# Kernel optimization log

Measured on AMD Instinct MI355X. Metric: run time of the kernel, lower is better.

Reference implementation:

```python
import jax, jax.numpy as jnp
import numpy as np

ALPHA = 0.05          # embed strength (frames in [0,1])
COEF_R, COEF_C = 4, 3 # mid-frequency DCT coefficient that carries the bit


def _dct_mat():
    # 8x8 orthonormal DCT-II matrix
    n = jnp.arange(8, dtype=jnp.float32)
    D = jnp.cos(jnp.pi * (2.0 * n[None, :] + 1.0) * n[:, None] / 16.0) * jnp.sqrt(2.0 / 8.0)
    return D.at[0].multiply(1.0 / jnp.sqrt(2.0))


def rgb_to_yuv(rgb):
    r, g, b = rgb[:, 0:1], rgb[:, 1:2], rgb[:, 2:3]
    y = 0.299 * r + 0.587 * g + 0.114 * b
    u = -0.147 * r - 0.289 * g + 0.436 * b
    v = 0.615 * r - 0.515 * g - 0.1 * b
    return jnp.concatenate([y, u, v], axis=1)


def yuv_to_rgb(yuv):
    y, u, v = yuv[:, 0:1], yuv[:, 1:2], yuv[:, 2:3]
    r = y + 1.14 * v
    g = y - 0.395 * u - 0.581 * v
    b = y + 2.032 * u
    return jnp.concatenate([r, g, b], axis=1)


def lbp_uniform(gray):
    # uniform LBP, P=8, R=1 (integer 8-neighborhood), per-image max-normalized
    B, H, W = gray.shape
    p = jnp.pad(gray, ((0, 0), (1, 1), (1, 1)), mode='edge')
    offs = [(-1, 0), (-1, 1), (0, 1), (1, 1), (1, 0), (1, -1), (0, -1), (-1, -1)]
    neigh = jnp.stack([p[:, 1 + dy:1 + dy + H, 1 + dx:1 + dx + W] for dy, dx in offs], axis=0)
    bits = (neigh >= gray[None]).astype(jnp.float32)          # [8,B,H,W]
    trans = jnp.sum(jnp.abs(bits - jnp.roll(bits, 1, axis=0)), axis=0)
    s = jnp.sum(bits, axis=0)
    code = jnp.where(trans <= 2.0, s, 9.0)
    mx = jnp.max(code, axis=(1, 2), keepdims=True)
    return code / mx                                           # [B,H,W]


def dct_embed(y, watermark, mask):
    # y: [B,H,W] luma; watermark: [L] int bits; mask: [B,H,W] texture strength
    B, H, W = y.shape
    nh, nw = H // 8, W // 8
    D = _dct_mat()
    yb = y.reshape(B, nh, 8, nw, 8).transpose(0, 1, 3, 2, 4)   # [B,nh,nw,8,8]
    coef = jnp.einsum('ij,bhwjk,lk->bhwil', D, yb, D)          # D @ block @ D^T
    strength = mask.reshape(B, nh, 8, nw, 8).mean(axis=(2, 4)) # [B,nh,nw]
    L = watermark.shape[0]
    idx = (jnp.arange(nh * nw) % L).reshape(nh, nw)
    bits = watermark[idx].astype(jnp.float32)                  # [nh,nw]
    delta = ALPHA * strength * (2.0 * bits - 1.0)[None]        # [B,nh,nw]
    coef = coef.at[..., COEF_R, COEF_C].add(delta)
    inv = jnp.einsum('ji,bhwjk,kl->bhwil', D, coef, D)         # D^T @ coef @ D
    return inv.transpose(0, 1, 3, 2, 4).reshape(B, H, W)


def _forward(frame, watermark, sa_w, sa_b, ca_w1, ca_w2):
    # LBP texture features from grayscale
    gray = 0.299 * frame[:, 0] + 0.587 * frame[:, 1] + 0.114 * frame[:, 2]
    lbp = lbp_uniform(gray)[:, None]                           # [B,1,H,W]
    # spatial attention: 7x7 conv over [frame, lbp] -> sigmoid mask
    sa_in = jnp.concatenate([frame, lbp], axis=1)
    mask = jax.nn.sigmoid(
        jax.lax.conv_general_dilated(sa_in, sa_w, (1, 1), 'SAME',
                                     dimension_numbers=('NCHW', 'OIHW', 'NCHW'))
        + sa_b[None, :, None, None])                           # [B,1,H,W]
    # channel attention on YUV
    yuv = rgb_to_yuv(frame)
    pooled = yuv.mean(axis=(2, 3))                             # [B,3]
    scale = jax.nn.sigmoid(jax.nn.relu(pooled @ ca_w1.T) @ ca_w2.T)
    weighted = yuv * scale[:, :, None, None]
    # blockwise DCT watermark embed on Y channel
    y_marked = dct_embed(weighted[:, 0], watermark, mask[:, 0])
    wm_yuv = jnp.concatenate([y_marked[:, None], weighted[:, 1:2], weighted[:, 2:3]], axis=1)
    return yuv_to_rgb(wm_yuv), mask


def setup_inputs() -> dict:
    key = jax.random.key(0)
    k1, k2, k3, k4, k5 = jax.random.split(key, 5)
    B, H, W, L = 16, 512, 512, 64
    frame = jax.random.uniform(k1, (B, 3, H, W), dtype=jnp.float32)
    watermark = jax.random.randint(k2, (L,), 0, 2, dtype=jnp.int32)
    sa_w = jax.random.normal(k3, (1, 4, 7, 7), dtype=jnp.float32) * 0.1
    sa_b = jnp.zeros((1,), dtype=jnp.float32)
    ca_w1 = jax.random.normal(k4, (3, 3), dtype=jnp.float32) * 0.5
    ca_w2 = jax.random.normal(k5, (3, 3), dtype=jnp.float32) * 0.5
    return {"frame": frame, "watermark": watermark, "sa_w": sa_w, "sa_b": sa_b,
            "ca_w1": ca_w1, "ca_w2": ca_w2}


def reference(frame, watermark, sa_w, sa_b, ca_w1, ca_w2):
    return _forward(frame, watermark, sa_w, sa_b, ca_w1, ca_w2)
```

## Files before the change

kernel.cpp:

```cpp
#include <hip/hip_runtime.h>
#include <stdint.h>

#define BB 16
#define HH 512
#define WW 512
#define HWsz (HH*WW)

__device__ __forceinline__ float grayf(float r,float g,float b){
  return __fadd_rn(__fadd_rn(__fmul_rn(0.299f,r),__fmul_rn(0.587f,g)),__fmul_rn(0.114f,b));
}
__device__ __forceinline__ float sigmoidf_(float x){ return 1.0f/(1.0f+expf(-x)); }

__device__ __forceinline__ int lbp_code(float tl,float tc,float tr,
                                        float ml,float c ,float mr,
                                        float bl,float bc,float br){
  int b0 = tc>=c, b1 = tr>=c, b2 = mr>=c, b3 = br>=c;
  int b4 = bc>=c, b5 = bl>=c, b6 = ml>=c, b7 = tl>=c;
  int s = (b0+b1)+(b2+b3)+(b4+b5)+(b6+b7);
  int tr_ = (b0!=b7)+(b1!=b0)+(b2!=b1)+(b3!=b2)+(b4!=b3)+(b5!=b4)+(b6!=b5)+(b7!=b6);
  return (tr_<=2)? s : 9;
}

__global__ void k_init(float* sums, int* maxc){
  int t = threadIdx.x;
  if(t < BB*3) sums[t] = 0.0f;
  if(t < BB) maxc[t] = 0;
}

#define RSTRIDE 520
__global__ __launch_bounds__(256,4) void k_reduce(const float* __restrict__ frame,
     float* __restrict__ sums, int* __restrict__ maxc){
  const int blk = blockIdx.x;
  const int b = blk >> 6;
  const int s = blk & 63;
  const int r0 = s*8;
  const float4* F = (const float4*)(frame + (size_t)b*3*HWsz);
  __shared__ float sg[10*RSTRIDE];
  const int tid = threadIdx.x;
  float sy=0.f, su=0.f, sv=0.f;
  #pragma unroll
  for(int k=0;k<5;k++){
    int j = tid + 256*k;
    int row = j >> 7;
    int c4  = j & 127;
    int gy  = min(max(r0-1+row,0),HH-1);
    int fi  = gy*128 + c4;
    float4 r4 = F[fi];
    float4 g4 = F[65536  + fi];
    float4 b4 = F[131072 + fi];
    float4 gr;
    gr.x = grayf(r4.x,g4.x,b4.x);
    gr.y = grayf(r4.y,g4.y,b4.y);
    gr.z = grayf(r4.z,g4.z,b4.z);
    gr.w = grayf(r4.w,g4.w,b4.w);
    *(float4*)&sg[row*RSTRIDE + 4 + 4*c4] = gr;
    if(c4==0)   sg[row*RSTRIDE + 3]   = gr.x;
    if(c4==127) sg[row*RSTRIDE + 516] = gr.w;
    if(row>=1 && row<=8){
      sy += (gr.x+gr.y)+(gr.z+gr.w);
      float rs_=(r4.x+r4.y)+(r4.z+r4.w), gs_=(g4.x+g4.y)+(g4.z+g4.w), bs_=(b4.x+b4.y)+(b4.z+b4.w);
      su += -0.147f*rs_ - 0.289f*gs_ + 0.436f*bs_;
      sv +=  0.615f*rs_ - 0.515f*gs_ - 0.1f*bs_;
    }
  }
  __syncthreads();
  int cm = 0;
  {
    const float* base = sg + (2*tid + 3);
    float t0=base[0], t1=base[1], t2=base[2], t3=base[3];
    float m0=base[RSTRIDE], m1=base[RSTRIDE+1], m2=base[RSTRIDE+2], m3=base[RSTRIDE+3];
    #pragma unroll
    for(int R=1;R<=8;R++){
      const float* brow = base + (R+1)*RSTRIDE;
      float b0=brow[0], b1=brow[1], b2=brow[2], b3=brow[3];
      cm = max(cm, lbp_code(t0,t1,t2, m0,m1,m2, b0,b1,b2));
      cm = max(cm, lbp_code(t1,t2,t3, m1,m2,m3, b1,b2,b3));
      t0=m0;t1=m1;t2=m2;t3=m3; m0=b0;m1=b1;m2=b2;m3=b3;
    }
  }
  #pragma unroll
  for(int off=32;off>=1;off>>=1){
    sy += __shfl_down(sy,off,64);
    su += __shfl_down(su,off,64);
    sv += __shfl_down(sv,off,64);
    cm = max(cm,__shfl_down(cm,off,64));
  }
  __shared__ float rs[3][4]; __shared__ int rm[4];
  int wave=tid>>6, lane=tid&63;
  if(lane==0){ rs[0][wave]=sy; rs[1][wave]=su; rs[2][wave]=sv; rm[wave]=cm; }
  __syncthreads();
  if(tid==0){
    atomicAdd(&sums[b*3+0], (rs[0][0]+rs[0][1])+(rs[0][2]+rs[0][3]));
    atomicAdd(&sums[b*3+1], (rs[1][0]+rs[1][1])+(rs[1][2]+rs[1][3]));
    atomicAdd(&sums[b*3+2], (rs[2][0]+rs[2][1])+(rs[2][2]+rs[2][3]));
    atomicMax(&maxc[b], max(max(rm[0],rm[1]),max(rm[2],rm[3])));
  }
}

__global__ void k_scale(const float* __restrict__ sums, const int* __restrict__ maxc,
    const float* __restrict__ w1, const float* __restrict__ w2,
    float* __restrict__ scale, float* __restrict__ mxf){
  int b = threadIdx.x;
  if(b >= BB) return;
  float p[3], h[3];
  for(int j=0;j<3;j++) p[j] = sums[b*3+j] * (1.0f/(float)HWsz);
  for(int i=0;i<3;i++){
    float a = p[0]*w1[i*3+0] + p[1]*w1[i*3+1] + p[2]*w1[i*3+2];
    h[i] = fmaxf(a, 0.0f);
  }
  for(int i=0;i<3;i++){
    float a = h[0]*w2[i*3+0] + h[1]*w2[i*3+1] + h[2]*w2[i*3+2];
    scale[b*3+i] = sigmoidf_(a);
  }
  mxf[b] = fmaxf((float)maxc[b], 1.0f);
}

#define SAS 73
__global__ __launch_bounds__(256,3) void k_main(const float* __restrict__ frame,
    const int* __restrict__ wm, const float* __restrict__ sa_w, const float* __restrict__ sa_b,
    const float* __restrict__ scalev, const float* __restrict__ mxf,
    float* __restrict__ out)
{
  const int b = blockIdx.z;
  const int tx0 = blockIdx.x*64, ty0 = blockIdx.y*32;
  const float* fr = frame + (size_t)b*3*HWsz;
  const float4* F4 = (const float4*)fr;

  __shared__ float sA[4][38][SAS];
  __shared__ float sgt[76];
  __shared__ float sgb[76];
  __shared__ float ssc[4];
  __shared__ float scodetab[12];

  const int tid = threadIdx.x;
  if(tid < 3)  ssc[tid] = scalev[b*3 + tid];
  if(tid == 3) ssc[3] = sa_b[0];
  if(tid < 10) scodetab[tid] = (float)tid / mxf[b];

  for(int s = tid; s < 720; s += 256){
    int ly = s / 18;
    int k  = s - ly*18;
    int gy = ty0 + ly - 4;
    int ry = min(max(gy,0),HH-1);
    int gx0 = tx0 + 4*k - 4;
    bool xin = (gx0 >= 0) && (gx0 <= WW-4);
    float4 r4, g4, b4;
    if(xin){
      int fi = ry*(WW/4) + (gx0>>2);
      r4 = F4[fi]; g4 = F4[65536 + fi]; b4 = F4[131072 + fi];
    } else {
      int cc = (gx0 < 0) ? 0 : (WW-1);
      float r = fr[ry*WW+cc], g = fr[HWsz+ry*WW+cc], bl = fr[2*HWsz+ry*WW+cc];
      r4 = make_float4(r,r,r,r); g4 = make_float4(g,g,g,g); b4 = make_float4(bl,bl,bl,bl);
    }
    float gr0 = grayf(r4.x,g4.x,b4.x), gr1 = grayf(r4.y,g4.y,b4.y),
          gr2 = grayf(r4.z,g4.z,b4.z), gr3 = grayf(r4.w,g4.w,b4.w);
    int cbase = 4*k;
    float* gp = (ly==0) ? &sgt[cbase] : ((ly==39) ? &sgb[cbase] : &sA[3][ly-1][cbase]);
    gp[0]=gr0; gp[1]=gr1; gp[2]=gr2; gp[3]=gr3;
    if(ly >= 1 && ly <= 38){
      float z = ((gy >= 0) && (gy < HH) && xin) ? 1.0f : 0.0f;
      float* rp = &sA[0][ly-1][cbase];
      rp[0]          =r4.x*z; rp[1]          =r4.y*z; rp[2]          =r4.z*z; rp[3]          =r4.w*z;
      rp[38*SAS+0]   =g4.x*z; rp[38*SAS+1]   =g4.y*z; rp[38*SAS+2]   =g4.z*z; rp[38*SAS+3]   =g4.w*z;
      rp[2*38*SAS+0] =b4.x*z; rp[2*38*SAS+1] =b4.y*z; rp[2*38*SAS+2] =b4.z*z; rp[2*38*SAS+3] =b4.w*z;
    }
  }
  __syncthreads();

  float lv[3][4];
  #pragma unroll
  for(int it=0; it<3; ++it){
    int s2 = tid + 256*it;
    if(s2 < 684){
      int lr = s2 / 18;
      int q  = s2 - lr*18;
      int lx0 = 4*q;
      const float* rowM = &sA[3][lr][0];
      const float* rowT = (lr==0)  ? sgt : &sA[3][lr-1][0];
      const float* rowB = (lr==37) ? sgb : &sA[3][lr+1][0];
      float t_[6], m_[6], b_[6];
      #pragma unroll
      for(int j=0;j<6;j++){
        int c = lx0 - 1 + j;
        t_[j]=rowT[c]; m_[j]=rowM[c]; b_[j]=rowB[c];
      }
      int gy = ty0 + lr - 3;
      bool rowin = (gy >= 0) && (gy < HH);
      #pragma unroll
      for(int j=0;j<4;j++){
        int lx = lx0 + j;
        int gx = tx0 + lx - 4;
        float v = 0.0f;
        if(rowin && lx >= 1 && lx <= 70 && gx >= 0 && gx < WW){
          float c = m_[j+1];
          int msk = ((t_[j+1]>=c)?1:0)   | ((t_[j+2]>=c)?2:0)  | ((m_[j+2]>=c)?4:0) |
                    ((b_[j+2]>=c)?8:0)   | ((b_[j+1]>=c)?16:0) | ((b_[j]>=c)?32:0)  |
                    ((m_[j]>=c)?64:0)    | ((t_[j]>=c)?128:0);
          int s8  = __popc(msk);
          int rot = ((msk<<1) | (msk>>7)) & 255;
          int tr_ = __popc(msk ^ rot);
          int code = (tr_ <= 2) ? s8 : 9;
          v = scodetab[code];
        }
        lv[it][j] = v;
      }
    }
  }
  __syncthreads();
  #pragma unroll
  for(int it=0; it<3; ++it){
    int s2 = tid + 256*it;
    if(s2 < 684){
      int lr = s2 / 18;
      int q  = s2 - lr*18;
      float* wp2 = &sA[3][lr][4*q];
      wp2[0]=lv[it][0]; wp2[1]=lv[it][1]; wp2[2]=lv[it][2]; wp2[3]=lv[it][3];
    }
  }
  __syncthreads();

  const int t  = tid & 7;
  const int ty = tid >> 3;
  float a0=ssc[3], a1=ssc[3], a2=ssc[3], a3=ssc[3];
  float a4=ssc[3], a5=ssc[3], a6=ssc[3], a7=ssc[3];
  for(int ci=0;ci<4;ci++){
    #pragma unroll
    for(int ky=0;ky<7;ky++){
      const float* rowp = &sA[ci][ty+ky][8*t];
      float win[14];
      #pragma unroll
      for(int w=0;w<14;w++) win[w]=rowp[1+w];
      const float* wr = &sa_w[ci*49 + ky*7];
      #pragma unroll
      for(int kx=0;kx<7;kx++){
        float wt = wr[kx];
        a0 += win[kx+0]*wt;
        a1 += win[kx+1]*wt;
        a2 += win[kx+2]*wt;
        a3 += win[kx+3]*wt;
        a4 += win[kx+4]*wt;
        a5 += win[kx+5]*wt;
        a6 += win[kx+6]*wt;
        a7 += win[kx+7]*wt;
      }
    }
  }
  float m[8];
  m[0]=sigmoidf_(a0); m[1]=sigmoidf_(a1); m[2]=sigmoidf_(a2); m[3]=sigmoidf_(a3);
  m[4]=sigmoidf_(a4); m[5]=sigmoidf_(a5); m[6]=sigmoidf_(a6); m[7]=sigmoidf_(a7);
  {
    size_t midx = (size_t)(3*BB)*HWsz + (size_t)b*HWsz + (size_t)(ty0+ty)*WW + (size_t)(tx0+8*t);
    *reinterpret_cast<float4*>(out + midx)     = make_float4(m[0],m[1],m[2],m[3]);
    *reinterpret_cast<float4*>(out + midx + 4) = make_float4(m[4],m[5],m[6],m[7]);
  }

  float part = ((m[0]+m[1])+(m[2]+m[3])) + ((m[4]+m[5])+(m[6]+m[7]));
  part += __shfl_xor(part, 8, 64);
  part += __shfl_xor(part, 16, 64);
  part += __shfl_xor(part, 32, 64);
  const float strength = part * (1.0f/64.0f);

  {
    const float sc0=ssc[0], sc1=ssc[1], sc2=ssc[2];
    const int bw = (tx0 + 8*t) >> 3;
    const float sgn = (float)(2*wm[bw]-1);
    const float d4 = (((ty+1)&2) ? -0.35355339059327373f : 0.35355339059327373f);
    const float delta = 0.05f * strength * sgn * d4;
    const float D3tab[8] = { 0.4157348061512726f,-0.0975451610080641f,-0.4903926402016152f,-0.2777851165098011f,
                             0.2777851165098011f, 0.4903926402016152f, 0.0975451610080641f,-0.4157348061512726f };
    float vr[8], vg[8], vb[8];
    #pragma unroll
    for(int j=0;j<8;j++){
      float r  = sA[0][ty+3][8*t+j+4];
      float g  = sA[1][ty+3][8*t+j+4];
      float bl = sA[2][ty+3][8*t+j+4];
      float yv = (0.299f*r + 0.587f*g + 0.114f*bl) * sc0;
      float uv = (-0.147f*r - 0.289f*g + 0.436f*bl) * sc1;
      float vv = ( 0.615f*r - 0.515f*g - 0.1f*bl) * sc2;
      float ym = yv + delta * D3tab[j];
      vr[j] = ym + 1.14f*vv;
      vg[j] = ym - 0.395f*uv - 0.581f*vv;
      vb[j] = ym + 2.032f*uv;
    }
    size_t base = (size_t)(ty0+ty)*WW + (size_t)(tx0+8*t);
    float* o0 = out + (size_t)(b*3+0)*HWsz + base;
    float* o1 = out + (size_t)(b*3+1)*HWsz + base;
    float* o2 = out + (size_t)(b*3+2)*HWsz + base;
    *reinterpret_cast<float4*>(o0)   = make_float4(vr[0],vr[1],vr[2],vr[3]);
    *reinterpret_cast<float4*>(o0+4) = make_float4(vr[4],vr[5],vr[6],vr[7]);
    *reinterpret_cast<float4*>(o1)   = make_float4(vg[0],vg[1],vg[2],vg[3]);
    *reinterpret_cast<float4*>(o1+4) = make_float4(vg[4],vg[5],vg[6],vg[7]);
    *reinterpret_cast<float4*>(o2)   = make_float4(vb[0],vb[1],vb[2],vb[3]);
    *reinterpret_cast<float4*>(o2+4) = make_float4(vb[4],vb[5],vb[6],vb[7]);
  }
}

extern "C" void kernel_launch(void* const* d_in, const int* in_sizes, int n_in,
                              void* d_out, int out_size, void* d_ws, size_t ws_size,
                              hipStream_t stream) {
  const float* frame = (const float*)d_in[0];
  const int*   wmark = (const int*)d_in[1];
  const float* sa_w  = (const float*)d_in[2];
  const float* sa_b  = (const float*)d_in[3];
  const float* ca_w1 = (const float*)d_in[4];
  const float* ca_w2 = (const float*)d_in[5];
  float* out = (float*)d_out;
  char* ws = (char*)d_ws;
  float* sums  = (float*)(ws);
  int*   maxc  = (int*)(ws + 192);
  float* scalev= (float*)(ws + 256);
  float* mxf   = (float*)(ws + 448);

  hipLaunchKernelGGL(k_init,  dim3(1),        dim3(64),  0, stream, sums, maxc);
  hipLaunchKernelGGL(k_reduce,dim3(1024),     dim3(256), 0, stream, frame, sums, maxc);
  hipLaunchKernelGGL(k_scale, dim3(1),        dim3(64),  0, stream, sums, maxc, ca_w1, ca_w2, scalev, mxf);
  hipLaunchKernelGGL(k_main,  dim3(8,16,16),  dim3(256), 0, stream, frame, wmark, sa_w, sa_b, scalev, mxf, out);
}
```

Measured before the change: 187.6 us.

## Remap 7x7 conv threads to column-per-thread, 8-row vertical bands

Each thread now owns one column and eight consecutive rows instead of eight horizontal pixels in one row. Every loaded row of 7 taps is reused across up to eight output rows, and the 8x8 block mean becomes a cheap shuffle over eight adjacent lanes. Shared-memory reads become consecutive across lanes, which avoids the stride-8 bank conflicts of the old mapping. In exchange, output stores shrink from float4 vectors to scalar stores, which stay coalesced across the wave, and more FMAs run per loaded value.

```diff
diff --git a/kernel.cpp b/kernel.cpp
--- a/kernel.cpp
+++ b/kernel.cpp
@@ -220,79 +220,76 @@
   }
   __syncthreads();
 
-  const int t  = tid & 7;
-  const int ty = tid >> 3;
-  float a0=ssc[3], a1=ssc[3], a2=ssc[3], a3=ssc[3];
-  float a4=ssc[3], a5=ssc[3], a6=ssc[3], a7=ssc[3];
+  const int x    = tid & 63;
+  const int band = tid >> 6;
+  const int r0s  = band*8;
+  float acc[8];
+  {
+    const float bias = ssc[3];
+    #pragma unroll
+    for(int r=0;r<8;r++) acc[r]=bias;
+  }
   for(int ci=0;ci<4;ci++){
-    #pragma unroll
-    for(int ky=0;ky<7;ky++){
-      const float* rowp = &sA[ci][ty+ky][8*t];
-      float win[14];
+    const float* chan = &sA[ci][0][0] + (r0s)*SAS + (x+1);
+    const float* wci  = &sa_w[ci*49];
+    #pragma unroll
+    for(int i=0;i<14;i++){
+      const float* rowp = chan + i*SAS;
+      float tap[7];
       #pragma unroll
-      for(int w=0;w<14;w++) win[w]=rowp[1+w];
-      const float* wr = &sa_w[ci*49 + ky*7];
+      for(int k=0;k<7;k++) tap[k]=rowp[k];
       #pragma unroll
-      for(int kx=0;kx<7;kx++){
-        float wt = wr[kx];
-        a0 += win[kx+0]*wt;
-        a1 += win[kx+1]*wt;
-        a2 += win[kx+2]*wt;
-        a3 += win[kx+3]*wt;
-        a4 += win[kx+4]*wt;
-        a5 += win[kx+5]*wt;
-        a6 += win[kx+6]*wt;
-        a7 += win[kx+7]*wt;
+      for(int r=0;r<8;r++){
+        const int ky = i - r;
+        if(ky >= 0 && ky <= 6){
+          const float* wr = wci + ky*7;
+          acc[r] += tap[0]*wr[0]+tap[1]*wr[1]+tap[2]*wr[2]+tap[3]*wr[3]
+                  + tap[4]*wr[4]+tap[5]*wr[5]+tap[6]*wr[6];
+        }
       }
     }
   }
   float m[8];
-  m[0]=sigmoidf_(a0); m[1]=sigmoidf_(a1); m[2]=sigmoidf_(a2); m[3]=sigmoidf_(a3);
-  m[4]=sigmoidf_(a4); m[5]=sigmoidf_(a5); m[6]=sigmoidf_(a6); m[7]=sigmoidf_(a7);
+  float msum = 0.f;
+  #pragma unroll
+  for(int r=0;r<8;r++){ m[r]=sigmoidf_(acc[r]); msum += m[r]; }
   {
-    size_t midx = (size_t)(3*BB)*HWsz + (size_t)b*HWsz + (size_t)(ty0+ty)*WW + (size_t)(tx0+8*t);
-    *reinterpret_cast<float4*>(out + midx)     = make_float4(m[0],m[1],m[2],m[3]);
-    *reinterpret_cast<float4*>(out + midx + 4) = make_float4(m[4],m[5],m[6],m[7]);
-  }
-
-  float part = ((m[0]+m[1])+(m[2]+m[3])) + ((m[4]+m[5])+(m[6]+m[7]));
-  part += __shfl_xor(part, 8, 64);
-  part += __shfl_xor(part, 16, 64);
-  part += __shfl_xor(part, 32, 64);
-  const float strength = part * (1.0f/64.0f);
+    size_t mbase = (size_t)(3*BB)*HWsz + (size_t)b*HWsz + (size_t)(ty0+r0s)*WW + (size_t)(tx0+x);
+    #pragma unroll
+    for(int r=0;r<8;r++) out[mbase + (size_t)r*WW] = m[r];
+  }
+
+  msum += __shfl_xor(msum, 1, 64);
+  msum += __shfl_xor(msum, 2, 64);
+  msum += __shfl_xor(msum, 4, 64);
+  const float strength = msum * (1.0f/64.0f);
 
   {
     const float sc0=ssc[0], sc1=ssc[1], sc2=ssc[2];
-    const int bw = (tx0 + 8*t) >> 3;
-    const float sgn = (float)(2*wm[bw]-1);
-    const float d4 = (((ty+1)&2) ? -0.35355339059327373f : 0.35355339059327373f);
-    const float delta = 0.05f * strength * sgn * d4;
+    const float sgn = (float)(2*wm[(tx0+x)>>3]-1);
     const float D3tab[8] = { 0.4157348061512726f,-0.0975451610080641f,-0.4903926402016152f,-0.2777851165098011f,
                              0.2777851165098011f, 0.4903926402016152f, 0.0975451610080641f,-0.4157348061512726f };
-    float vr[8], vg[8], vb[8];
-    #pragma unroll
-    for(int j=0;j<8;j++){
-      float r  = sA[0][ty+3][8*t+j+4];
-      float g  = sA[1][ty+3][8*t+j+4];
-      float bl = sA[2][ty+3][8*t+j+4];
-      float yv = (0.299f*r + 0.587f*g + 0.114f*bl) * sc0;
-      float uv = (-0.147f*r - 0.289f*g + 0.436f*bl) * sc1;
-      float vv = ( 0.615f*r - 0.515f*g - 0.1f*bl) * sc2;
-      float ym = yv + delta * D3tab[j];
-      vr[j] = ym + 1.14f*vv;
-      vg[j] = ym - 0.395f*uv - 0.581f*vv;
-      vb[j] = ym + 2.032f*uv;
-    }
-    size_t base = (size_t)(ty0+ty)*WW + (size_t)(tx0+8*t);
-    float* o0 = out + (size_t)(b*3+0)*HWsz + base;
-    float* o1 = out + (size_t)(b*3+1)*HWsz + base;
-    float* o2 = out + (size_t)(b*3+2)*HWsz + base;
-    *reinterpret_cast<float4*>(o0)   = make_float4(vr[0],vr[1],vr[2],vr[3]);
-    *reinterpret_cast<float4*>(o0+4) = make_float4(vr[4],vr[5],vr[6],vr[7]);
-    *reinterpret_cast<float4*>(o1)   = make_float4(vg[0],vg[1],vg[2],vg[3]);
-    *reinterpret_cast<float4*>(o1+4) = make_float4(vg[4],vg[5],vg[6],vg[7]);
-    *reinterpret_cast<float4*>(o2)   = make_float4(vb[0],vb[1],vb[2],vb[3]);
-    *reinterpret_cast<float4*>(o2+4) = make_float4(vb[4],vb[5],vb[6],vb[7]);
+    const float dcol = D3tab[x & 7];
+    #pragma unroll
+    for(int r=0;r<8;r++){
+      const int rl = r0s + r;
+      float rr = sA[0][rl+3][x+4];
+      float gg = sA[1][rl+3][x+4];
+      float bb = sA[2][rl+3][x+4];
+      float yv = (0.299f*rr + 0.587f*gg + 0.114f*bb) * sc0;
+      float uv = (-0.147f*rr - 0.289f*gg + 0.436f*bb) * sc1;
+      float vv = ( 0.615f*rr - 0.515f*gg - 0.1f*bb) * sc2;
+      float d4 = (((rl+1)&2) ? -0.35355339059327373f : 0.35355339059327373f);
+      float delta = 0.05f * strength * sgn * d4;
+      float ym = yv + delta * dcol;
+      float vr = ym + 1.14f*vv;
+      float vg = ym - 0.395f*uv - 0.581f*vv;
+      float vb = ym + 2.032f*uv;
+      size_t base = (size_t)(ty0+rl)*WW + (size_t)(tx0+x);
+      out[(size_t)(b*3+0)*HWsz + base] = vr;
+      out[(size_t)(b*3+1)*HWsz + base] = vg;
+      out[(size_t)(b*3+2)*HWsz + base] = vb;
+    }
   }
 }
 
```

After: 190.4 us. No clear change (+1.5%).
